# Kernel optimization log

Hardware: AMD Instinct MI355X
Metric: run time of the kernel (lower is better)

## Reference

```python
import jax, jax.numpy as jnp
import numpy as np

N = 100000      # nodes
E = 1600000     # edges (avg degree 16)
H = 128         # hidden channels
L = 5           # num_layers (only valid range 4<num_layers<8 for this module; 4 index-errors)
ALPHA = 0.1
THETA = 0.5
EPS = 1e-5      # BatchNorm1d default eps


def setup_inputs() -> dict:
    key = jax.random.key(0)
    ks = jax.random.split(key, 8)
    x = jax.random.normal(ks[0], (N, H), dtype=jnp.float32)
    W_in = jax.random.normal(ks[1], (H, H), dtype=jnp.float32) / np.float32(np.sqrt(H))
    b_in = jnp.zeros((H,), jnp.float32)
    conv_W = jax.random.normal(ks[2], (L, H, H), dtype=jnp.float32) / np.float32(np.sqrt(H))
    bn_gamma = jnp.ones((L - 1, H), jnp.float32)
    bn_beta = jnp.zeros((L - 1, H), jnp.float32)
    W_jk = jax.random.normal(ks[3], (4 * H, H), dtype=jnp.float32) / np.float32(np.sqrt(4 * H))
    b_jk = jnp.zeros((H,), jnp.float32)
    src = jax.random.randint(ks[4], (E,), 0, N, dtype=jnp.int32).astype(jnp.int64)
    dst = jax.random.randint(ks[5], (E,), 0, N, dtype=jnp.int32).astype(jnp.int64)
    return dict(x=x, W_in=W_in, b_in=b_in, conv_W=conv_W, bn_gamma=bn_gamma,
                bn_beta=bn_beta, W_jk=W_jk, b_jk=b_jk, src=src, dst=dst)


def _batchnorm(z, gamma, beta):
    # BatchNorm1d, training-mode batch statistics over the node dimension
    m = z.mean(axis=0)
    v = z.var(axis=0)
    return (z - m) * jax.lax.rsqrt(v + EPS) * gamma + beta


def reference(x, W_in, b_in, conv_W, bn_gamma, bn_beta, W_jk, b_jk, src, dst):
    # lins[0]
    z = x @ W_in + b_in          # [N, H]
    x0 = z                       # initial residual for GCNII
    zs = []
    for i in range(L):
        # GCN2Conv (shared_weights=True, normalize=False):
        #   msg = A @ z  (sparse propagation over edge list)
        msg = jax.ops.segment_sum(z[src], dst, num_segments=N)   # [N, H]
        h = (1.0 - ALPHA) * msg + ALPHA * x0
        beta_l = float(np.log(THETA / (i + 1) + 1.0))
        z = (1.0 - beta_l) * h + beta_l * (h @ conv_W[i])
        zs.append(z)
        if i % 4 == 3:
            # JumpingKnowledge('cat') over the 4 layer outputs, then lins[-1].
            # (Original code also applies BN here but immediately overwrites z,
            #  so that BN is dead computation and is skipped.)
            z = jnp.concatenate(zs[:4], axis=-1) @ W_jk + b_jk   # [N, H]
        elif i < L - 1:
            z = jax.nn.relu(_batchnorm(z, bn_gamma[i], bn_beta[i]))
    return z
```

## Files before the change

kernel.cpp:

```cpp
#include <hip/hip_runtime.h>
#include <hip/hip_bf16.h>
#include <cmath>
#include <cstddef>

#define NN 100000
#define HH 128
#define EE 1600000
#define NH (NN * HH)
#define ALPHA_C 0.1f
#define THETA_C 0.5f
#define EPS_C 1e-5f

constexpr int TR = 64;
constexpr int AST = 68;
constexpr int SCAN_B = 256;
constexpr int NBLK = (NN + SCAN_B - 1) / SCAN_B;

__global__ __launch_bounds__(256) void zero_int_k(int* __restrict__ p, int n) {
    int i = blockIdx.x * 256 + threadIdx.x;
    if (i < n) p[i] = 0;
}
__global__ __launch_bounds__(256) void zero_f4_k(float4* __restrict__ p, int n4) {
    int i = blockIdx.x * 256 + threadIdx.x;
    if (i < n4) p[i] = float4{0.f, 0.f, 0.f, 0.f};
}

__global__ void detect_idx64(const int* __restrict__ p, int* __restrict__ flag) {
    int any = 0;
    for (int i = 0; i < 64; ++i) any |= p[2 * i + 1];
    *flag = (any == 0) ? 1 : 0;
}

__device__ __forceinline__ int load_idx(const void* p, int e, int is64) {
    return is64 ? (int)((const long long*)p)[e] : ((const int*)p)[e];
}

__global__ __launch_bounds__(256) void hist_k(
    const void* __restrict__ dstp, const int* __restrict__ flag,
    int* __restrict__ hist)
{
    int e = blockIdx.x * 256 + threadIdx.x;
    if (e >= EE) return;
    atomicAdd(&hist[load_idx(dstp, e, *flag)], 1);
}

__global__ __launch_bounds__(SCAN_B) void scan1_k(
    const int* __restrict__ hist, int* __restrict__ incl, int* __restrict__ bsum)
{
    __shared__ int sh[SCAN_B];
    int t = threadIdx.x;
    int i = blockIdx.x * SCAN_B + t;
    int v = (i < NN) ? hist[i] : 0;
    sh[t] = v;
    __syncthreads();
    for (int off = 1; off < SCAN_B; off <<= 1) {
        int x = (t >= off) ? sh[t - off] : 0;
        __syncthreads();
        sh[t] += x;
        __syncthreads();
    }
    if (i < NN) incl[i] = sh[t];
    if (t == SCAN_B - 1) bsum[blockIdx.x] = sh[t];
}

__global__ __launch_bounds__(512) void scan2_k(int* __restrict__ bsum) {
    __shared__ int sh[512];
    int t = threadIdx.x;
    sh[t] = (t < NBLK) ? bsum[t] : 0;
    __syncthreads();
    for (int off = 1; off < 512; off <<= 1) {
        int x = (t >= off) ? sh[t - off] : 0;
        __syncthreads();
        sh[t] += x;
        __syncthreads();
    }
    if (t < NBLK) bsum[t] = sh[t];
}

__global__ __launch_bounds__(SCAN_B) void scan3_k(
    const int* __restrict__ hist, const int* __restrict__ incl,
    const int* __restrict__ bsum, int* __restrict__ row_ptr,
    int* __restrict__ cursor)
{
    int b = blockIdx.x;
    int i = b * SCAN_B + threadIdx.x;
    if (i < NN) {
        int ex = incl[i] - hist[i] + (b > 0 ? bsum[b - 1] : 0);
        row_ptr[i] = ex;
        cursor[i] = ex;
    }
    if (i == 0) row_ptr[NN] = EE;
}

__global__ __launch_bounds__(256) void fill_k(
    const void* __restrict__ srcp, const void* __restrict__ dstp,
    const int* __restrict__ flag, int* __restrict__ cursor,
    int* __restrict__ sorted_src)
{
    int e = blockIdx.x * 256 + threadIdx.x;
    if (e >= EE) return;
    int is64 = *flag;
    int d = load_idx(dstp, e, is64);
    int pos = atomicAdd(&cursor[d], 1);
    sorted_src[pos] = load_idx(srcp, e, is64);
}

__global__ __launch_bounds__(256) void gather_k(
    const float* __restrict__ z, const int* __restrict__ row_ptr,
    const int* __restrict__ sorted_src,
    const float* __restrict__ stats,
    const float* __restrict__ gamma, const float* __restrict__ beta,
    const float* __restrict__ resid,
    float* __restrict__ msg)
{
    int node = blockIdx.x * 4 + (threadIdx.x >> 6);
    if (node >= NN) return;
    int lane = threadIdx.x & 63;
    int half = lane >> 5;
    int c4 = lane & 31;

    float4 r4 = ((const float4*)(resid + (size_t)node * HH))[c4];

    const bool bn = (stats != nullptr);
    float4 sc = {1.f, 1.f, 1.f, 1.f}, sh = {0.f, 0.f, 0.f, 0.f};
    if (bn) {
        const float invN = 1.f / (float)NN;
        float4 s  = ((const float4*)stats)[c4];
        float4 s2 = ((const float4*)(stats + 128))[c4];
        float4 g  = ((const float4*)gamma)[c4];
        float4 b  = ((const float4*)beta)[c4];
        float m, var;
        m = s.x * invN; var = s2.x * invN - m * m;
        sc.x = rsqrtf(var + EPS_C) * g.x; sh.x = b.x - m * sc.x;
        m = s.y * invN; var = s2.y * invN - m * m;
        sc.y = rsqrtf(var + EPS_C) * g.y; sh.y = b.y - m * sc.y;
        m = s.z * invN; var = s2.z * invN - m * m;
        sc.z = rsqrtf(var + EPS_C) * g.z; sh.z = b.z - m * sc.z;
        m = s.w * invN; var = s2.w * invN - m * m;
        sc.w = rsqrtf(var + EPS_C) * g.w; sh.w = b.w - m * sc.w;
    }

    int e1 = row_ptr[node + 1];
    int e = row_ptr[node] + half;
    float4 acc  = {0.f, 0.f, 0.f, 0.f};
    float4 acc2 = {0.f, 0.f, 0.f, 0.f};
    float4 acc3 = {0.f, 0.f, 0.f, 0.f};
    float4 acc4 = {0.f, 0.f, 0.f, 0.f};
    for (; e + 6 < e1; e += 8) {
        int s0 = sorted_src[e];
        int s1 = sorted_src[e + 2];
        int s2 = sorted_src[e + 4];
        int s3 = sorted_src[e + 6];
        float4 v0 = ((const float4*)(z + (size_t)s0 * HH))[c4];
        float4 v1 = ((const float4*)(z + (size_t)s1 * HH))[c4];
        float4 v2 = ((const float4*)(z + (size_t)s2 * HH))[c4];
        float4 v3 = ((const float4*)(z + (size_t)s3 * HH))[c4];
        if (bn) {
            v0.x = fmaxf(0.f, v0.x * sc.x + sh.x);
            v0.y = fmaxf(0.f, v0.y * sc.y + sh.y);
            v0.z = fmaxf(0.f, v0.z * sc.z + sh.z);
            v0.w = fmaxf(0.f, v0.w * sc.w + sh.w);
            v1.x = fmaxf(0.f, v1.x * sc.x + sh.x);
            v1.y = fmaxf(0.f, v1.y * sc.y + sh.y);
            v1.z = fmaxf(0.f, v1.z * sc.z + sh.z);
            v1.w = fmaxf(0.f, v1.w * sc.w + sh.w);
            v2.x = fmaxf(0.f, v2.x * sc.x + sh.x);
            v2.y = fmaxf(0.f, v2.y * sc.y + sh.y);
            v2.z = fmaxf(0.f, v2.z * sc.z + sh.z);
            v2.w = fmaxf(0.f, v2.w * sc.w + sh.w);
            v3.x = fmaxf(0.f, v3.x * sc.x + sh.x);
            v3.y = fmaxf(0.f, v3.y * sc.y + sh.y);
            v3.z = fmaxf(0.f, v3.z * sc.z + sh.z);
            v3.w = fmaxf(0.f, v3.w * sc.w + sh.w);
        }
        acc.x  += v0.x; acc.y  += v0.y; acc.z  += v0.z; acc.w  += v0.w;
        acc2.x += v1.x; acc2.y += v1.y; acc2.z += v1.z; acc2.w += v1.w;
        acc3.x += v2.x; acc3.y += v2.y; acc3.z += v2.z; acc3.w += v2.w;
        acc4.x += v3.x; acc4.y += v3.y; acc4.z += v3.z; acc4.w += v3.w;
    }
    for (; e + 2 < e1; e += 4) {
        int s0 = sorted_src[e];
        int s1 = sorted_src[e + 2];
        float4 v0 = ((const float4*)(z + (size_t)s0 * HH))[c4];
        float4 v1 = ((const float4*)(z + (size_t)s1 * HH))[c4];
        if (bn) {
            v0.x = fmaxf(0.f, v0.x * sc.x + sh.x);
            v0.y = fmaxf(0.f, v0.y * sc.y + sh.y);
            v0.z = fmaxf(0.f, v0.z * sc.z + sh.z);
            v0.w = fmaxf(0.f, v0.w * sc.w + sh.w);
            v1.x = fmaxf(0.f, v1.x * sc.x + sh.x);
            v1.y = fmaxf(0.f, v1.y * sc.y + sh.y);
            v1.z = fmaxf(0.f, v1.z * sc.z + sh.z);
            v1.w = fmaxf(0.f, v1.w * sc.w + sh.w);
        }
        acc.x  += v0.x; acc.y  += v0.y; acc.z  += v0.z; acc.w  += v0.w;
        acc2.x += v1.x; acc2.y += v1.y; acc2.z += v1.z; acc2.w += v1.w;
    }
    if (e < e1) {
        int s = sorted_src[e];
        float4 v = ((const float4*)(z + (size_t)s * HH))[c4];
        if (bn) {
            v.x = fmaxf(0.f, v.x * sc.x + sh.x);
            v.y = fmaxf(0.f, v.y * sc.y + sh.y);
            v.z = fmaxf(0.f, v.z * sc.z + sh.z);
            v.w = fmaxf(0.f, v.w * sc.w + sh.w);
        }
        acc.x += v.x; acc.y += v.y; acc.z += v.z; acc.w += v.w;
    }
    acc.x += acc2.x + acc3.x + acc4.x;
    acc.y += acc2.y + acc3.y + acc4.y;
    acc.z += acc2.z + acc3.z + acc4.z;
    acc.w += acc2.w + acc3.w + acc4.w;
    acc.x += __shfl_down(acc.x, 32);
    acc.y += __shfl_down(acc.y, 32);
    acc.z += __shfl_down(acc.z, 32);
    acc.w += __shfl_down(acc.w, 32);
    if (half == 0) {
        const float cA = 1.f - ALPHA_C, cB = ALPHA_C;
        float4 o = {cA * acc.x + cB * r4.x, cA * acc.y + cB * r4.y,
                    cA * acc.z + cB * r4.z, cA * acc.w + cB * r4.w};
        ((float4*)(msg + (size_t)node * HH))[c4] = o;
    }
}

__global__ __launch_bounds__(256) void prep_w(
    const float* __restrict__ W_in, const float* __restrict__ conv_W,
    float* __restrict__ Wp)
{
    int i = blockIdx.y;
    int idx = blockIdx.x * 256 + threadIdx.x;
    float v;
    if (i == 0) {
        v = W_in[idx];
    } else {
        float bl = logf(THETA_C / (float)i + 1.f);
        int k = idx >> 7, c = idx & 127;
        v = bl * conv_W[(size_t)(i - 1) * 16384 + idx] + ((k == c) ? (1.f - bl) : 0.f);
    }
    Wp[(size_t)i * 16384 + idx] = v;
}

__global__ __launch_bounds__(256, 4) void gemm128(
    const float* __restrict__ A, const float* __restrict__ Wp,
    const float* __restrict__ bias, float* __restrict__ out,
    float* __restrict__ statsp, int nrows)
{
    __shared__ float As[HH * AST];
    const int t = threadIdx.x;
    const int tx = t & 31;
    const int ty = t >> 5;
    const int lane = t & 63, w = t >> 6;
    const int row0 = blockIdx.x * TR;

#pragma unroll
    for (int i = 0; i < 8; ++i) {
        int r = (i & 3) * 16 + (lane & 15);
        int k4 = ((i >> 2) * 4 + w) * 4 + (lane >> 4);
        float4 v = {0.f, 0.f, 0.f, 0.f};
        if (row0 + r < nrows)
            v = ((const float4*)(A + (size_t)(row0 + r) * HH))[k4];
        int k = k4 * 4;
        As[(k + 0) * AST + r] = v.x;
        As[(k + 1) * AST + r] = v.y;
        As[(k + 2) * AST + r] = v.z;
        As[(k + 3) * AST + r] = v.w;
    }
    __syncthreads();

    float acc[8][4];
#pragma unroll
    for (int ii = 0; ii < 8; ++ii)
#pragma unroll
        for (int j = 0; j < 4; ++j) acc[ii][j] = 0.f;

    const float4* W4 = (const float4*)Wp;
    float4 wbuf[4];
#pragma unroll
    for (int kk = 0; kk < 4; ++kk) wbuf[kk] = W4[kk * 32 + tx];

    for (int k0 = 0; k0 < HH; k0 += 4) {
        float4 wn[4];
        const bool more = (k0 + 4 < HH);
#pragma unroll
        for (int kk = 0; kk < 4; ++kk) {
            if (more) wn[kk] = W4[(k0 + 4 + kk) * 32 + tx];
            int k = k0 + kk;
            const float* ap = &As[k * AST + ty * 8];
            float4 a0 = *(const float4*)ap;
            float4 a1 = *(const float4*)(ap + 4);
            float a[8] = {a0.x, a0.y, a0.z, a0.w, a1.x, a1.y, a1.z, a1.w};
#pragma unroll
            for (int ii = 0; ii < 8; ++ii) {
                acc[ii][0] += a[ii] * wbuf[kk].x;
                acc[ii][1] += a[ii] * wbuf[kk].y;
                acc[ii][2] += a[ii] * wbuf[kk].z;
                acc[ii][3] += a[ii] * wbuf[kk].w;
            }
        }
        if (more) {
#pragma unroll
            for (int kk = 0; kk < 4; ++kk) wbuf[kk] = wn[kk];
        }
    }

    float4 b4 = {0.f, 0.f, 0.f, 0.f};
    if (bias) b4 = ((const float4*)bias)[tx];
    float cs[4] = {0.f, 0.f, 0.f, 0.f}, cq[4] = {0.f, 0.f, 0.f, 0.f};
    const bool doStats = (statsp != nullptr);
#pragma unroll
    for (int ii = 0; ii < 8; ++ii) {
        int r = row0 + ty * 8 + ii;
        if (r < nrows) {
            float4 v = {acc[ii][0] + b4.x, acc[ii][1] + b4.y,
                        acc[ii][2] + b4.z, acc[ii][3] + b4.w};
            ((float4*)out)[(size_t)r * 32 + tx] = v;
            if (doStats) {
                cs[0] += v.x; cq[0] += v.x * v.x;
                cs[1] += v.y; cq[1] += v.y * v.y;
                cs[2] += v.z; cq[2] += v.z * v.z;
                cs[3] += v.w; cq[3] += v.w * v.w;
            }
        }
    }
    if (doStats) {
        __syncthreads();
        float* red = As;
#pragma unroll
        for (int j = 0; j < 4; ++j) {
            red[ty * 128 + tx * 4 + j] = cs[j];
            red[1024 + ty * 128 + tx * 4 + j] = cq[j];
        }
        __syncthreads();
        if (t < 128) {
            float s = 0.f, q = 0.f;
#pragma unroll
            for (int g = 0; g < 8; ++g) {
                s += red[g * 128 + t];
                q += red[1024 + g * 128 + t];
            }
            atomicAdd(&statsp[t], s);
            atomicAdd(&statsp[128 + t], q);
        }
    }
}

__global__ __launch_bounds__(256, 4) void gemm_jk(
    const float* __restrict__ z0, const float* __restrict__ z1,
    const float* __restrict__ z2, const float* __restrict__ z3,
    const float* __restrict__ Wjk, const float* __restrict__ bjk,
    float* __restrict__ out, int nrows)
{
    __shared__ float As[HH * AST];
    const int t = threadIdx.x;
    const int tx = t & 31;
    const int ty = t >> 5;
    const int lane = t & 63, w = t >> 6;
    const int row0 = blockIdx.x * TR;

    float acc[8][4];
#pragma unroll
    for (int ii = 0; ii < 8; ++ii)
#pragma unroll
        for (int j = 0; j < 4; ++j) acc[ii][j] = 0.f;

    const float* srcs[4] = {z0, z1, z2, z3};
    for (int j = 0; j < 4; ++j) {
        if (j) __syncthreads();
        const float* Z = srcs[j];
#pragma unroll
        for (int i = 0; i < 8; ++i) {
            int r = (i & 3) * 16 + (lane & 15);
            int k4 = ((i >> 2) * 4 + w) * 4 + (lane >> 4);
            float4 v = {0.f, 0.f, 0.f, 0.f};
            if (row0 + r < nrows)
                v = ((const float4*)(Z + (size_t)(row0 + r) * HH))[k4];
            int k = k4 * 4;
            As[(k + 0) * AST + r] = v.x;
            As[(k + 1) * AST + r] = v.y;
            As[(k + 2) * AST + r] = v.z;
            As[(k + 3) * AST + r] = v.w;
        }
        __syncthreads();

        const float4* W4 = (const float4*)(Wjk + (size_t)j * 128 * HH);
        float4 wbuf[4];
#pragma unroll
        for (int kk = 0; kk < 4; ++kk) wbuf[kk] = W4[kk * 32 + tx];

        for (int k0 = 0; k0 < HH; k0 += 4) {
            float4 wn[4];
            const bool more = (k0 + 4 < HH);
#pragma unroll
            for (int kk = 0; kk < 4; ++kk) {
                if (more) wn[kk] = W4[(k0 + 4 + kk) * 32 + tx];
                int k = k0 + kk;
                const float* ap = &As[k * AST + ty * 8];
                float4 a0 = *(const float4*)ap;
                float4 a1 = *(const float4*)(ap + 4);
                float a[8] = {a0.x, a0.y, a0.z, a0.w, a1.x, a1.y, a1.z, a1.w};
#pragma unroll
                for (int ii = 0; ii < 8; ++ii) {
                    acc[ii][0] += a[ii] * wbuf[kk].x;
                    acc[ii][1] += a[ii] * wbuf[kk].y;
                    acc[ii][2] += a[ii] * wbuf[kk].z;
                    acc[ii][3] += a[ii] * wbuf[kk].w;
                }
            }
            if (more) {
#pragma unroll
                for (int kk = 0; kk < 4; ++kk) wbuf[kk] = wn[kk];
            }
        }
    }

    float4 b4 = ((const float4*)bjk)[tx];
#pragma unroll
    for (int ii = 0; ii < 8; ++ii) {
        int r = row0 + ty * 8 + ii;
        if (r < nrows) {
            float4 v = {acc[ii][0] + b4.x, acc[ii][1] + b4.y,
                        acc[ii][2] + b4.z, acc[ii][3] + b4.w};
            ((float4*)out)[(size_t)r * 32 + tx] = v;
        }
    }
}

extern "C" void kernel_launch(void* const* d_in, const int* in_sizes, int n_in,
                              void* d_out, int out_size, void* d_ws, size_t ws_size,
                              hipStream_t stream)
{
    const float* x       = (const float*)d_in[0];
    const float* W_in    = (const float*)d_in[1];
    const float* b_in    = (const float*)d_in[2];
    const float* conv_W  = (const float*)d_in[3];
    const float* bn_g    = (const float*)d_in[4];
    const float* bn_b    = (const float*)d_in[5];
    const float* W_jk    = (const float*)d_in[6];
    const float* b_jk    = (const float*)d_in[7];
    const void*  srcp    = d_in[8];
    const void*  dstp    = d_in[9];

    float* ws     = (float*)d_ws;
    float* x0     = ws;
    float* msg    = ws + (size_t)NH;
    float* zs0    = ws + 2 * (size_t)NH;
    float* zs1    = ws + 3 * (size_t)NH;
    float* zs2    = ws + 4 * (size_t)NH;
    float* stats3 = ws + 5 * (size_t)NH;
    int*   flag       = (int*)(stats3 + 768);
    int*   hist       = flag + 1;
    int*   incl       = hist + NN;
    int*   row_ptr    = incl + NN;
    int*   cursor     = row_ptr + NN + 1;
    int*   bsum       = cursor + NN;
    int*   sorted_src = bsum + NBLK + 1;
    float* Wp         = (float*)(sorted_src + EE);

    const int GEMM_GRID = (NN + TR - 1) / TR;
    const int EDGE_GRID = (EE + 255) / 256;
    const int NODE_GRID = (NN + 3) / 4;

    detect_idx64<<<1, 1, 0, stream>>>((const int*)srcp, flag);
    zero_int_k<<<(NN + 255) / 256, 256, 0, stream>>>(hist, NN);
    zero_f4_k<<<1, 192, 0, stream>>>((float4*)stats3, 192);
    hist_k<<<EDGE_GRID, 256, 0, stream>>>(dstp, flag, hist);
    scan1_k<<<NBLK, SCAN_B, 0, stream>>>(hist, incl, bsum);
    scan2_k<<<1, 512, 0, stream>>>(bsum);
    scan3_k<<<NBLK, SCAN_B, 0, stream>>>(hist, incl, bsum, row_ptr, cursor);
    fill_k<<<EDGE_GRID, 256, 0, stream>>>(srcp, dstp, flag, cursor, sorted_src);
    prep_w<<<dim3(64, 6), 256, 0, stream>>>(W_in, conv_W, Wp);

    gemm128<<<GEMM_GRID, 256, 0, stream>>>(x, Wp, b_in, x0, nullptr, NN);

    const float* act = x0;
    const float* stats_cur = nullptr;
    const float* g_cur = nullptr;
    const float* b_cur = nullptr;

    for (int i = 0; i < 5; ++i) {
        gather_k<<<NODE_GRID, 256, 0, stream>>>(act, row_ptr, sorted_src,
                                                stats_cur, g_cur, b_cur, x0, msg);

        float* zraw = (i >= 3) ? (float*)d_out : (zs0 + (size_t)i * NH);
        float* stats_next = (i < 3) ? (stats3 + (size_t)i * 256) : nullptr;
        gemm128<<<GEMM_GRID, 256, 0, stream>>>(msg, Wp + (size_t)(i + 1) * 16384,
                                               nullptr, zraw, stats_next, NN);
        if (i < 3) {
            act = zraw;
            stats_cur = stats_next;
            g_cur = bn_g + (size_t)i * HH;
            b_cur = bn_b + (size_t)i * HH;
        } else if (i == 3) {
            gemm_jk<<<GEMM_GRID, 256, 0, stream>>>(zs0, zs1, zs2,
                                                   (const float*)d_out, W_jk, b_jk,
                                                   zs0, NN);
            act = zs0;
            stats_cur = nullptr;
            g_cur = nullptr;
            b_cur = nullptr;
        }
    }
}
```

Baseline: 1.519 ms.

## Fuse edge gather with per-layer GEMM, keeping aggregated rows in shared memory

Each GCN2 layer now runs one kernel instead of two. That kernel gathers the neighbour sums for a 64-node tile, applies the BN/ReLU and residual mix, and writes the result straight into shared memory, then runs the 128x128 GEMM and the stats reduction on it. This removes the round trip of the intermediate msg buffer through global memory and one launch per layer. In exchange, each wave gathers 16 nodes in sequence and occupancy is limited by the larger block footprint, which can hurt latency hiding on the random gathers.

```diff
diff --git a/kernel.cpp b/kernel.cpp
--- a/kernel.cpp
+++ b/kernel.cpp
@@ -105,25 +105,122 @@
     sorted_src[pos] = load_idx(srcp, e, is64);
 }
 
-__global__ __launch_bounds__(256) void gather_k(
+__global__ __launch_bounds__(256) void prep_w(
+    const float* __restrict__ W_in, const float* __restrict__ conv_W,
+    float* __restrict__ Wp)
+{
+    int i = blockIdx.y;
+    int idx = blockIdx.x * 256 + threadIdx.x;
+    float v;
+    if (i == 0) {
+        v = W_in[idx];
+    } else {
+        float bl = logf(THETA_C / (float)i + 1.f);
+        int k = idx >> 7, c = idx & 127;
+        v = bl * conv_W[(size_t)(i - 1) * 16384 + idx] + ((k == c) ? (1.f - bl) : 0.f);
+    }
+    Wp[(size_t)i * 16384 + idx] = v;
+}
+
+__global__ __launch_bounds__(256, 4) void gemm128(
+    const float* __restrict__ A, const float* __restrict__ Wp,
+    const float* __restrict__ bias, float* __restrict__ out,
+    float* __restrict__ statsp, int nrows)
+{
+    __shared__ float As[HH * AST];
+    const int t = threadIdx.x;
+    const int tx = t & 31;
+    const int ty = t >> 5;
+    const int lane = t & 63, w = t >> 6;
+    const int row0 = blockIdx.x * TR;
+
+#pragma unroll
+    for (int i = 0; i < 8; ++i) {
+        int r = (i & 3) * 16 + (lane & 15);
+        int k4 = ((i >> 2) * 4 + w) * 4 + (lane >> 4);
+        float4 v = {0.f, 0.f, 0.f, 0.f};
+        if (row0 + r < nrows)
+            v = ((const float4*)(A + (size_t)(row0 + r) * HH))[k4];
+        int k = k4 * 4;
+        As[(k + 0) * AST + r] = v.x;
+        As[(k + 1) * AST + r] = v.y;
+        As[(k + 2) * AST + r] = v.z;
+        As[(k + 3) * AST + r] = v.w;
+    }
+    __syncthreads();
+
+    float acc[8][4];
+#pragma unroll
+    for (int ii = 0; ii < 8; ++ii)
+#pragma unroll
+        for (int j = 0; j < 4; ++j) acc[ii][j] = 0.f;
+
+    const float4* W4 = (const float4*)Wp;
+    float4 wbuf[4];
+#pragma unroll
+    for (int kk = 0; kk < 4; ++kk) wbuf[kk] = W4[kk * 32 + tx];
+
+    for (int k0 = 0; k0 < HH; k0 += 4) {
+        float4 wn[4];
+        const bool more = (k0 + 4 < HH);
+#pragma unroll
+        for (int kk = 0; kk < 4; ++kk) {
+            if (more) wn[kk] = W4[(k0 + 4 + kk) * 32 + tx];
+            int k = k0 + kk;
+            const float* ap = &As[k * AST + ty * 8];
+            float4 a0 = *(const float4*)ap;
+            float4 a1 = *(const float4*)(ap + 4);
+            float a[8] = {a0.x, a0.y, a0.z, a0.w, a1.x, a1.y, a1.z, a1.w};
+#pragma unroll
+            for (int ii = 0; ii < 8; ++ii) {
+                acc[ii][0] += a[ii] * wbuf[kk].x;
+                acc[ii][1] += a[ii] * wbuf[kk].y;
+                acc[ii][2] += a[ii] * wbuf[kk].z;
+                acc[ii][3] += a[ii] * wbuf[kk].w;
+            }
+        }
+        if (more) {
+#pragma unroll
+            for (int kk = 0; kk < 4; ++kk) wbuf[kk] = wn[kk];
+        }
+    }
+
+    float4 b4 = {0.f, 0.f, 0.f, 0.f};
+    if (bias) b4 = ((const float4*)bias)[tx];
+#pragma unroll
+    for (int ii = 0; ii < 8; ++ii) {
+        int r = row0 + ty * 8 + ii;
+        if (r < nrows) {
+            float4 v = {acc[ii][0] + b4.x, acc[ii][1] + b4.y,
+                        acc[ii][2] + b4.z, acc[ii][3] + b4.w};
+            ((float4*)out)[(size_t)r * 32 + tx] = v;
+        }
+    }
+    (void)statsp;
+}
+
+template <bool BN, bool DOSTATS>
+__global__ __launch_bounds__(256, 2) void fused_layer(
     const float* __restrict__ z, const int* __restrict__ row_ptr,
     const int* __restrict__ sorted_src,
     const float* __restrict__ stats,
     const float* __restrict__ gamma, const float* __restrict__ beta,
     const float* __restrict__ resid,
-    float* __restrict__ msg)
-{
-    int node = blockIdx.x * 4 + (threadIdx.x >> 6);
-    if (node >= NN) return;
-    int lane = threadIdx.x & 63;
-    int half = lane >> 5;
-    int c4 = lane & 31;
-
-    float4 r4 = ((const float4*)(resid + (size_t)node * HH))[c4];
-
-    const bool bn = (stats != nullptr);
+    const float* __restrict__ Wp, float* __restrict__ out,
+    float* __restrict__ statsp, int nrows)
+{
+    __shared__ float As[HH * AST];
+    const int t = threadIdx.x;
+    const int tx = t & 31;
+    const int ty = t >> 5;
+    const int lane = t & 63, w = t >> 6;
+    const int row0 = blockIdx.x * TR;
+
+    const int half = lane >> 5;
+    const int c4 = lane & 31;
+
     float4 sc = {1.f, 1.f, 1.f, 1.f}, sh = {0.f, 0.f, 0.f, 0.f};
-    if (bn) {
+    if (BN) {
         const float invN = 1.f / (float)NN;
         float4 s  = ((const float4*)stats)[c4];
         float4 s2 = ((const float4*)(stats + 128))[c4];
@@ -140,130 +237,95 @@
         sc.w = rsqrtf(var + EPS_C) * g.w; sh.w = b.w - m * sc.w;
     }
 
-    int e1 = row_ptr[node + 1];
-    int e = row_ptr[node] + half;
-    float4 acc  = {0.f, 0.f, 0.f, 0.f};
-    float4 acc2 = {0.f, 0.f, 0.f, 0.f};
-    float4 acc3 = {0.f, 0.f, 0.f, 0.f};
-    float4 acc4 = {0.f, 0.f, 0.f, 0.f};
-    for (; e + 6 < e1; e += 8) {
-        int s0 = sorted_src[e];
-        int s1 = sorted_src[e + 2];
-        int s2 = sorted_src[e + 4];
-        int s3 = sorted_src[e + 6];
-        float4 v0 = ((const float4*)(z + (size_t)s0 * HH))[c4];
-        float4 v1 = ((const float4*)(z + (size_t)s1 * HH))[c4];
-        float4 v2 = ((const float4*)(z + (size_t)s2 * HH))[c4];
-        float4 v3 = ((const float4*)(z + (size_t)s3 * HH))[c4];
-        if (bn) {
-            v0.x = fmaxf(0.f, v0.x * sc.x + sh.x);
-            v0.y = fmaxf(0.f, v0.y * sc.y + sh.y);
-            v0.z = fmaxf(0.f, v0.z * sc.z + sh.z);
-            v0.w = fmaxf(0.f, v0.w * sc.w + sh.w);
-            v1.x = fmaxf(0.f, v1.x * sc.x + sh.x);
-            v1.y = fmaxf(0.f, v1.y * sc.y + sh.y);
-            v1.z = fmaxf(0.f, v1.z * sc.z + sh.z);
-            v1.w = fmaxf(0.f, v1.w * sc.w + sh.w);
-            v2.x = fmaxf(0.f, v2.x * sc.x + sh.x);
-            v2.y = fmaxf(0.f, v2.y * sc.y + sh.y);
-            v2.z = fmaxf(0.f, v2.z * sc.z + sh.z);
-            v2.w = fmaxf(0.f, v2.w * sc.w + sh.w);
-            v3.x = fmaxf(0.f, v3.x * sc.x + sh.x);
-            v3.y = fmaxf(0.f, v3.y * sc.y + sh.y);
-            v3.z = fmaxf(0.f, v3.z * sc.z + sh.z);
-            v3.w = fmaxf(0.f, v3.w * sc.w + sh.w);
-        }
-        acc.x  += v0.x; acc.y  += v0.y; acc.z  += v0.z; acc.w  += v0.w;
-        acc2.x += v1.x; acc2.y += v1.y; acc2.z += v1.z; acc2.w += v1.w;
-        acc3.x += v2.x; acc3.y += v2.y; acc3.z += v2.z; acc3.w += v2.w;
-        acc4.x += v3.x; acc4.y += v3.y; acc4.z += v3.z; acc4.w += v3.w;
-    }
-    for (; e + 2 < e1; e += 4) {
-        int s0 = sorted_src[e];
-        int s1 = sorted_src[e + 2];
-        float4 v0 = ((const float4*)(z + (size_t)s0 * HH))[c4];
-        float4 v1 = ((const float4*)(z + (size_t)s1 * HH))[c4];
-        if (bn) {
-            v0.x = fmaxf(0.f, v0.x * sc.x + sh.x);
-            v0.y = fmaxf(0.f, v0.y * sc.y + sh.y);
-            v0.z = fmaxf(0.f, v0.z * sc.z + sh.z);
-            v0.w = fmaxf(0.f, v0.w * sc.w + sh.w);
-            v1.x = fmaxf(0.f, v1.x * sc.x + sh.x);
-            v1.y = fmaxf(0.f, v1.y * sc.y + sh.y);
-            v1.z = fmaxf(0.f, v1.z * sc.z + sh.z);
-            v1.w = fmaxf(0.f, v1.w * sc.w + sh.w);
-        }
-        acc.x  += v0.x; acc.y  += v0.y; acc.z  += v0.z; acc.w  += v0.w;
-        acc2.x += v1.x; acc2.y += v1.y; acc2.z += v1.z; acc2.w += v1.w;
-    }
-    if (e < e1) {
-        int s = sorted_src[e];
-        float4 v = ((const float4*)(z + (size_t)s * HH))[c4];
-        if (bn) {
-            v.x = fmaxf(0.f, v.x * sc.x + sh.x);
-            v.y = fmaxf(0.f, v.y * sc.y + sh.y);
-            v.z = fmaxf(0.f, v.z * sc.z + sh.z);
-            v.w = fmaxf(0.f, v.w * sc.w + sh.w);
-        }
-        acc.x += v.x; acc.y += v.y; acc.z += v.z; acc.w += v.w;
-    }
-    acc.x += acc2.x + acc3.x + acc4.x;
-    acc.y += acc2.y + acc3.y + acc4.y;
-    acc.z += acc2.z + acc3.z + acc4.z;
-    acc.w += acc2.w + acc3.w + acc4.w;
-    acc.x += __shfl_down(acc.x, 32);
-    acc.y += __shfl_down(acc.y, 32);
-    acc.z += __shfl_down(acc.z, 32);
-    acc.w += __shfl_down(acc.w, 32);
-    if (half == 0) {
-        const float cA = 1.f - ALPHA_C, cB = ALPHA_C;
-        float4 o = {cA * acc.x + cB * r4.x, cA * acc.y + cB * r4.y,
-                    cA * acc.z + cB * r4.z, cA * acc.w + cB * r4.w};
-        ((float4*)(msg + (size_t)node * HH))[c4] = o;
-    }
-}
-
-__global__ __launch_bounds__(256) void prep_w(
-    const float* __restrict__ W_in, const float* __restrict__ conv_W,
-    float* __restrict__ Wp)
-{
-    int i = blockIdx.y;
-    int idx = blockIdx.x * 256 + threadIdx.x;
-    float v;
-    if (i == 0) {
-        v = W_in[idx];
-    } else {
-        float bl = logf(THETA_C / (float)i + 1.f);
-        int k = idx >> 7, c = idx & 127;
-        v = bl * conv_W[(size_t)(i - 1) * 16384 + idx] + ((k == c) ? (1.f - bl) : 0.f);
-    }
-    Wp[(size_t)i * 16384 + idx] = v;
-}
-
-__global__ __launch_bounds__(256, 4) void gemm128(
-    const float* __restrict__ A, const float* __restrict__ Wp,
-    const float* __restrict__ bias, float* __restrict__ out,
-    float* __restrict__ statsp, int nrows)
-{
-    __shared__ float As[HH * AST];
-    const int t = threadIdx.x;
-    const int tx = t & 31;
-    const int ty = t >> 5;
-    const int lane = t & 63, w = t >> 6;
-    const int row0 = blockIdx.x * TR;
-
-#pragma unroll
-    for (int i = 0; i < 8; ++i) {
-        int r = (i & 3) * 16 + (lane & 15);
-        int k4 = ((i >> 2) * 4 + w) * 4 + (lane >> 4);
-        float4 v = {0.f, 0.f, 0.f, 0.f};
-        if (row0 + r < nrows)
-            v = ((const float4*)(A + (size_t)(row0 + r) * HH))[k4];
-        int k = k4 * 4;
-        As[(k + 0) * AST + r] = v.x;
-        As[(k + 1) * AST + r] = v.y;
-        As[(k + 2) * AST + r] = v.z;
-        As[(k + 3) * AST + r] = v.w;
+    for (int i = 0; i < 16; ++i) {
+        int rr = w * 16 + i;
+        int node = row0 + rr;
+        if (node < nrows) {
+            float4 r4v = ((const float4*)(resid + (size_t)node * HH))[c4];
+            int e1 = row_ptr[node + 1];
+            int e = row_ptr[node] + half;
+            float4 acc  = {0.f, 0.f, 0.f, 0.f};
+            float4 acc2 = {0.f, 0.f, 0.f, 0.f};
+            float4 acc3 = {0.f, 0.f, 0.f, 0.f};
+            float4 acc4 = {0.f, 0.f, 0.f, 0.f};
+            for (; e + 6 < e1; e += 8) {
+                int s0 = sorted_src[e];
+                int s1 = sorted_src[e + 2];
+                int s2 = sorted_src[e + 4];
+                int s3 = sorted_src[e + 6];
+                float4 v0 = ((const float4*)(z + (size_t)s0 * HH))[c4];
+                float4 v1 = ((const float4*)(z + (size_t)s1 * HH))[c4];
+                float4 v2 = ((const float4*)(z + (size_t)s2 * HH))[c4];
+                float4 v3 = ((const float4*)(z + (size_t)s3 * HH))[c4];
+                if (BN) {
+                    v0.x = fmaxf(0.f, v0.x * sc.x + sh.x);
+                    v0.y = fmaxf(0.f, v0.y * sc.y + sh.y);
+                    v0.z = fmaxf(0.f, v0.z * sc.z + sh.z);
+                    v0.w = fmaxf(0.f, v0.w * sc.w + sh.w);
+                    v1.x = fmaxf(0.f, v1.x * sc.x + sh.x);
+                    v1.y = fmaxf(0.f, v1.y * sc.y + sh.y);
+                    v1.z = fmaxf(0.f, v1.z * sc.z + sh.z);
+                    v1.w = fmaxf(0.f, v1.w * sc.w + sh.w);
+                    v2.x = fmaxf(0.f, v2.x * sc.x + sh.x);
+                    v2.y = fmaxf(0.f, v2.y * sc.y + sh.y);
+                    v2.z = fmaxf(0.f, v2.z * sc.z + sh.z);
+                    v2.w = fmaxf(0.f, v2.w * sc.w + sh.w);
+                    v3.x = fmaxf(0.f, v3.x * sc.x + sh.x);
+                    v3.y = fmaxf(0.f, v3.y * sc.y + sh.y);
+                    v3.z = fmaxf(0.f, v3.z * sc.z + sh.z);
+                    v3.w = fmaxf(0.f, v3.w * sc.w + sh.w);
+                }
+                acc.x  += v0.x; acc.y  += v0.y; acc.z  += v0.z; acc.w  += v0.w;
+                acc2.x += v1.x; acc2.y += v1.y; acc2.z += v1.z; acc2.w += v1.w;
+                acc3.x += v2.x; acc3.y += v2.y; acc3.z += v2.z; acc3.w += v2.w;
+                acc4.x += v3.x; acc4.y += v3.y; acc4.z += v3.z; acc4.w += v3.w;
+            }
+            for (; e + 2 < e1; e += 4) {
+                int s0 = sorted_src[e];
+                int s1 = sorted_src[e + 2];
+                float4 v0 = ((const float4*)(z + (size_t)s0 * HH))[c4];
+                float4 v1 = ((const float4*)(z + (size_t)s1 * HH))[c4];
+                if (BN) {
+                    v0.x = fmaxf(0.f, v0.x * sc.x + sh.x);
+                    v0.y = fmaxf(0.f, v0.y * sc.y + sh.y);
+                    v0.z = fmaxf(0.f, v0.z * sc.z + sh.z);
+                    v0.w = fmaxf(0.f, v0.w * sc.w + sh.w);
+                    v1.x = fmaxf(0.f, v1.x * sc.x + sh.x);
+                    v1.y = fmaxf(0.f, v1.y * sc.y + sh.y);
+                    v1.z = fmaxf(0.f, v1.z * sc.z + sh.z);
+                    v1.w = fmaxf(0.f, v1.w * sc.w + sh.w);
+                }
+                acc.x  += v0.x; acc.y  += v0.y; acc.z  += v0.z; acc.w  += v0.w;
+                acc2.x += v1.x; acc2.y += v1.y; acc2.z += v1.z; acc2.w += v1.w;
+            }
+            if (e < e1) {
+                int s = sorted_src[e];
+                float4 v = ((const float4*)(z + (size_t)s * HH))[c4];
+                if (BN) {
+                    v.x = fmaxf(0.f, v.x * sc.x + sh.x);
+                    v.y = fmaxf(0.f, v.y * sc.y + sh.y);
+                    v.z = fmaxf(0.f, v.z * sc.z + sh.z);
+                    v.w = fmaxf(0.f, v.w * sc.w + sh.w);
+                }
+                acc.x += v.x; acc.y += v.y; acc.z += v.z; acc.w += v.w;
+            }
+            acc.x += acc2.x + acc3.x + acc4.x;
+            acc.y += acc2.y + acc3.y + acc4.y;
+            acc.z += acc2.z + acc3.z + acc4.z;
+            acc.w += acc2.w + acc3.w + acc4.w;
+            acc.x += __shfl_down(acc.x, 32);
+            acc.y += __shfl_down(acc.y, 32);
+            acc.z += __shfl_down(acc.z, 32);
+            acc.w += __shfl_down(acc.w, 32);
+            if (half == 0) {
+                const float cA = 1.f - ALPHA_C, cB = ALPHA_C;
+                int k = c4 * 4;
+                As[(k + 0) * AST + rr] = cA * acc.x + cB * r4v.x;
+                As[(k + 1) * AST + rr] = cA * acc.y + cB * r4v.y;
+                As[(k + 2) * AST + rr] = cA * acc.z + cB * r4v.z;
+                As[(k + 3) * AST + rr] = cA * acc.w + cB * r4v.w;
+            }
+        }
     }
     __syncthreads();
 
@@ -303,18 +365,14 @@
         }
     }
 
-    float4 b4 = {0.f, 0.f, 0.f, 0.f};
-    if (bias) b4 = ((const float4*)bias)[tx];
     float cs[4] = {0.f, 0.f, 0.f, 0.f}, cq[4] = {0.f, 0.f, 0.f, 0.f};
-    const bool doStats = (statsp != nullptr);
 #pragma unroll
     for (int ii = 0; ii < 8; ++ii) {
         int r = row0 + ty * 8 + ii;
         if (r < nrows) {
-            float4 v = {acc[ii][0] + b4.x, acc[ii][1] + b4.y,
-                        acc[ii][2] + b4.z, acc[ii][3] + b4.w};
+            float4 v = {acc[ii][0], acc[ii][1], acc[ii][2], acc[ii][3]};
             ((float4*)out)[(size_t)r * 32 + tx] = v;
-            if (doStats) {
+            if (DOSTATS) {
                 cs[0] += v.x; cq[0] += v.x * v.x;
                 cs[1] += v.y; cq[1] += v.y * v.y;
                 cs[2] += v.z; cq[2] += v.z * v.z;
@@ -322,7 +380,7 @@
             }
         }
     }
-    if (doStats) {
+    if (DOSTATS) {
         __syncthreads();
         float* red = As;
 #pragma unroll
@@ -455,10 +513,10 @@
     int*   bsum       = cursor + NN;
     int*   sorted_src = bsum + NBLK + 1;
     float* Wp         = (float*)(sorted_src + EE);
+    (void)msg;
 
     const int GEMM_GRID = (NN + TR - 1) / TR;
     const int EDGE_GRID = (EE + 255) / 256;
-    const int NODE_GRID = (NN + 3) / 4;
 
     detect_idx64<<<1, 1, 0, stream>>>((const int*)srcp, flag);
     zero_int_k<<<(NN + 255) / 256, 256, 0, stream>>>(hist, NN);
@@ -472,32 +530,21 @@
 
     gemm128<<<GEMM_GRID, 256, 0, stream>>>(x, Wp, b_in, x0, nullptr, NN);
 
-    const float* act = x0;
-    const float* stats_cur = nullptr;
-    const float* g_cur = nullptr;
-    const float* b_cur = nullptr;
-
-    for (int i = 0; i < 5; ++i) {
-        gather_k<<<NODE_GRID, 256, 0, stream>>>(act, row_ptr, sorted_src,
-                                                stats_cur, g_cur, b_cur, x0, msg);
-
-        float* zraw = (i >= 3) ? (float*)d_out : (zs0 + (size_t)i * NH);
-        float* stats_next = (i < 3) ? (stats3 + (size_t)i * 256) : nullptr;
-        gemm128<<<GEMM_GRID, 256, 0, stream>>>(msg, Wp + (size_t)(i + 1) * 16384,
-                                               nullptr, zraw, stats_next, NN);
-        if (i < 3) {
-            act = zraw;
-            stats_cur = stats_next;
-            g_cur = bn_g + (size_t)i * HH;
-            b_cur = bn_b + (size_t)i * HH;
-        } else if (i == 3) {
-            gemm_jk<<<GEMM_GRID, 256, 0, stream>>>(zs0, zs1, zs2,
-                                                   (const float*)d_out, W_jk, b_jk,
-                                                   zs0, NN);
-            act = zs0;
-            stats_cur = nullptr;
-            g_cur = nullptr;
-            b_cur = nullptr;
-        }
-    }
-}
+    fused_layer<false, true><<<GEMM_GRID, 256, 0, stream>>>(
+        x0, row_ptr, sorted_src, nullptr, nullptr, nullptr, x0,
+        Wp + 1 * 16384, zs0, stats3 + 0, NN);
+    fused_layer<true, true><<<GEMM_GRID, 256, 0, stream>>>(
+        zs0, row_ptr, sorted_src, stats3 + 0, bn_g + 0, bn_b + 0, x0,
+        Wp + 2 * 16384, zs1, stats3 + 256, NN);
+    fused_layer<true, true><<<GEMM_GRID, 256, 0, stream>>>(
+        zs1, row_ptr, sorted_src, stats3 + 256, bn_g + HH, bn_b + HH, x0,
+        Wp + 3 * 16384, zs2, stats3 + 512, NN);
+    fused_layer<true, false><<<GEMM_GRID, 256, 0, stream>>>(
+        zs2, row_ptr, sorted_src, stats3 + 512, bn_g + 2 * HH, bn_b + 2 * HH, x0,
+        Wp + 4 * 16384, (float*)d_out, nullptr, NN);
+    gemm_jk<<<GEMM_GRID, 256, 0, stream>>>(zs0, zs1, zs2, (const float*)d_out,
+                                           W_jk, b_jk, zs0, NN);
+    fused_layer<false, false><<<GEMM_GRID, 256, 0, stream>>>(
+        zs0, row_ptr, sorted_src, nullptr, nullptr, nullptr, x0,
+        Wp + 5 * 16384, (float*)d_out, nullptr, NN);
+}
```

Result: faster. 1.435 ms (-5.6%).
